# Optimization experiments

Measured on AMD Instinct MI355X. Metric: run time of the kernel, lower is better.

Reference implementation:

```python
import jax, jax.numpy as jnp
import numpy as np

B, S, D, H = 2, 2048, 1024, 16
DK = D // H


def setup_inputs() -> dict:
    key = jax.random.key(0)
    ks = jax.random.split(key, 14)
    inp = {
        'query': jax.random.normal(ks[0], (B, S, D), jnp.float32),
        'key': jax.random.normal(ks[1], (B, S, D), jnp.float32),
        'value': jax.random.normal(ks[2], (B, S, D), jnp.float32),
        'mask': jax.random.randint(ks[3], (B, 1, S, S), 0, 2).astype(bool),
        'rel_pos_bias': jax.random.normal(ks[4], (1, H, S, S), jnp.float32),
    }
    scale = 1.0 / np.sqrt(D)
    names = ['Wq', 'bq', 'Wk', 'bk', 'Wv', 'bv', 'Wo', 'bo']
    for i, n in enumerate(names):
        k = ks[5 + i]
        if n.startswith('W'):
            inp[n] = jax.random.normal(k, (D, D), jnp.float32) * scale
        else:
            inp[n] = jnp.zeros((D,), jnp.float32)
    return inp


def reference(query, key, value, mask, rel_pos_bias, Wq, bq, Wk, bk, Wv, bv, Wo, bo):
    # torch Linear: y = x @ W^T + b; W stored [out, in]
    def proj(x, W, b):
        y = x @ W.T + b                       # [B,S,D]
        return y.reshape(B, S, H, DK).transpose(0, 2, 1, 3)  # [B,H,S,DK]

    q = proj(query, Wq, bq)
    k = proj(key, Wk, bk)
    v = proj(value, Wv, bv)

    scores = jnp.einsum('bhqd,bhkd->bhqk', q, k) / jnp.sqrt(jnp.float32(DK))
    scores = scores + rel_pos_bias
    scores = jnp.where(mask, jnp.float32(-1e9), scores)
    p_attn = jax.nn.softmax(scores, axis=-1)
    x = jnp.einsum('bhqk,bhkd->bhqd', p_attn, v)  # [B,H,S,DK]
    x = x.transpose(0, 2, 1, 3).reshape(B, S, D)
    return x @ Wo.T + bo
```

## Files before the change

kernel.cpp:

```cpp
#include <hip/hip_runtime.h>
#include <stdint.h>


typedef _Float16 f16;
typedef _Float16 f16x8 __attribute__((ext_vector_type(8)));
typedef _Float16 f16x4 __attribute__((ext_vector_type(4)));
typedef float f32x4 __attribute__((ext_vector_type(4)));

#define LOG2E 1.44269504088896340736f

__device__ __forceinline__ void gload16(const void* g, void* l) {
  __builtin_amdgcn_global_load_lds(
      (const __attribute__((address_space(1))) unsigned int*)g,
      (__attribute__((address_space(3))) unsigned int*)l, 16, 0, 0);
}

__global__ __launch_bounds__(256) void cvt_f32_f16(const float* __restrict__ in,
                                                   f16* __restrict__ out, int n4) {
  const int i = blockIdx.x * 256 + threadIdx.x;
  if (i >= n4) return;
  const float4 v = ((const float4*)in)[i];
  f16x4 o = {(f16)v.x, (f16)v.y, (f16)v.z, (f16)v.w};
  ((f16x4*)out)[i] = o;
}

__global__ void mask_detect(const uint8_t* __restrict__ m, int* __restrict__ flag) {
  __shared__ int s_off, s_weird;
  const int t = threadIdx.x;
  if (t == 0) { s_off = 0; s_weird = 0; }
  __syncthreads();
  int f_off = 0, f_weird = 0;
  for (int i = t; i < 8192; i += 256) {
    const uint8_t v = m[i];
    if ((i & 3) && v) f_off = 1;
    if (v > 1) f_weird = 1;
  }
  if (f_off) atomicOr(&s_off, 1);
  if (f_weird) atomicOr(&s_weird, 1);
  __syncthreads();
  if (t == 0) *flag = (s_off && !s_weird) ? 1 : 0;
}

__global__ __launch_bounds__(256) void mask_canon(const uint8_t* __restrict__ m,
                                                  uint8_t* __restrict__ out,
                                                  const int* __restrict__ flag) {
  const int i = (blockIdx.x * 256 + threadIdx.x) * 4;
  uchar4 o;
  if (*flag) {
    const uchar4 v = *(const uchar4*)(m + i);
    o = make_uchar4(v.x != 0, v.y != 0, v.z != 0, v.w != 0);
  } else {
    const int4 v = *(const int4*)((const int*)m + i);
    o = make_uchar4(v.x != 0, v.y != 0, v.z != 0, v.w != 0);
  }
  *(uchar4*)(out + i) = o;
}

template <int MODE>
__global__ __launch_bounds__(256, 2) void gemm_bt(const f16* __restrict__ A,
                                                  const f16* __restrict__ Bw,
                                                  const float* __restrict__ bias,
                                                  void* __restrict__ outp,
                                                  float scale) {
  constexpr int K = 1024;
  const int t = threadIdx.x;
  const int w = t >> 6, lane = t & 63, l15 = lane & 15, l4 = lane >> 4;
  const int bm = (int)(blockIdx.x >> 4) * 128;
  const int bn = (int)(blockIdx.x & 15) * 64;

  __shared__ f16 As[2][128 * 32];
  __shared__ f16 Bs[2][64 * 32];

  const f16* a0 = A + (size_t)(bm + (t >> 2)) * K + (t & 3) * 8;
  const f16* a1 = a0 + (size_t)64 * K;
  const f16* b0 = Bw + (size_t)(bn + (t >> 2)) * K + (t & 3) * 8;

  f32x4 acc[2][4];
#pragma unroll
  for (int m = 0; m < 2; ++m)
#pragma unroll
    for (int n = 0; n < 4; ++n) acc[m][n] = (f32x4){0.f, 0.f, 0.f, 0.f};

#define STAGE_G(buf, k0)                          \
  do {                                            \
    gload16(a0 + (k0), &As[buf][w * 512]);        \
    gload16(a1 + (k0), &As[buf][2048 + w * 512]); \
    gload16(b0 + (k0), &Bs[buf][w * 512]);        \
  } while (0)

  STAGE_G(0, 0);
  __syncthreads();
  int cur = 0;
#pragma unroll 1
  for (int kt = 0; kt < 32; ++kt) {
    if (kt < 31) STAGE_G(cur ^ 1, (kt + 1) * 32);
    const f16* ap = &As[cur][(w * 32 + l15) * 32 + l4 * 8];
    const f16* bp = &Bs[cur][l15 * 32 + l4 * 8];
    f16x8 af[2], bfr[4];
#pragma unroll
    for (int m = 0; m < 2; ++m) af[m] = *(const f16x8*)(ap + m * 512);
#pragma unroll
    for (int n = 0; n < 4; ++n) bfr[n] = *(const f16x8*)(bp + n * 512);
#pragma unroll
    for (int m = 0; m < 2; ++m)
#pragma unroll
      for (int n = 0; n < 4; ++n)
        acc[m][n] = __builtin_amdgcn_mfma_f32_16x16x32_f16(af[m], bfr[n], acc[m][n], 0, 0, 0);
    __syncthreads();
    cur ^= 1;
  }
#undef STAGE_G

#pragma unroll
  for (int m = 0; m < 2; ++m) {
    const int r0 = bm + w * 32 + m * 16 + (l4 << 2);
#pragma unroll
    for (int n = 0; n < 4; ++n) {
      const int c = bn + n * 16 + l15;
      const float bv = bias[c];
#pragma unroll
      for (int j = 0; j < 4; ++j) {
        const int r = r0 + j;
        const float v = (acc[m][n][j] + bv) * scale;
        if (MODE == 0) {
          const int b_ = r >> 11, s = r & 2047, h_ = c >> 6, dk = c & 63;
          ((f16*)outp)[(((size_t)b_ * 16 + h_) * 2048 + s) * 64 + dk] = (f16)v;
        } else if (MODE == 1) {
          const int b_ = r >> 11, s = r & 2047, h_ = c >> 6, dk = c & 63;
          ((f16*)outp)[(((size_t)b_ * 16 + h_) * 64 + dk) * 2048 + s] = (f16)v;
        } else {
          ((float*)outp)[(size_t)r * 1024 + c] = v;
        }
      }
    }
  }
}

__device__ __forceinline__ const f16x8* swzr(const f16* base, int row, int bytecol) {
  return (const f16x8*)((const char*)base + row * 128 + (bytecol ^ ((row & 7) << 4)));
}

__global__ __launch_bounds__(256, 4) void attn_fwd(
    const f16* __restrict__ Qp, const f16* __restrict__ Kp,
    const f16* __restrict__ Vt, const float* __restrict__ bias,
    const uint8_t* __restrict__ mask, f16* __restrict__ X) {
  constexpr int S = 2048;
  const int bid = blockIdx.x;
  const int qt = bid & 31, b = (bid >> 5) & 1, h = bid >> 6;
  const int t = threadIdx.x, w = t >> 6, lane = t & 63;
  const int l15 = lane & 15, l4 = lane >> 4;
  const int q0 = qt * 64 + w * 16;

  const f16* Qbh = Qp + (size_t)(b * 16 + h) * S * 64;
  const f16* Kbh = Kp + (size_t)(b * 16 + h) * S * 64;
  const f16* Vbh = Vt + (size_t)(b * 16 + h) * 64 * S;
  const float* biasr = bias + (size_t)h * S * S + (size_t)(q0 + l15) * S + l4 * 4;
  const uint8_t* maskr = mask + (size_t)b * S * S + (size_t)(q0 + l15) * S + l4 * 4;

  __shared__ f16 Ks[2][64 * 64];
  __shared__ f16 Vs[2][64 * 64];
  __shared__ f16 Ps[4][16 * 64];

  f16x8 qf[2];
#pragma unroll
  for (int ks = 0; ks < 2; ++ks)
    qf[ks] = *(const f16x8*)(Qbh + (size_t)(q0 + l15) * 64 + ks * 32 + l4 * 8);

  f32x4 oacc[4];
#pragma unroll
  for (int n = 0; n < 4; ++n) oacc[n] = (f32x4){0.f, 0.f, 0.f, 0.f};
  float mrow = -3e38f, lrow = 0.f;

  const int srow = t >> 3;
  const int scol = (((t & 7) ^ (srow & 7)) << 3);

#define STAGE(bf, kk)                                                              \
  do {                                                                             \
    gload16(Kbh + (size_t)((kk) + srow) * 64 + scol, &Ks[bf][w * 512]);            \
    gload16(Kbh + (size_t)((kk) + 32 + srow) * 64 + scol, &Ks[bf][2048 + w * 512]);\
    gload16(Vbh + (size_t)srow * S + (kk) + scol, &Vs[bf][w * 512]);               \
    gload16(Vbh + (size_t)(32 + srow) * S + (kk) + scol, &Vs[bf][2048 + w * 512]); \
  } while (0)

  STAGE(0, 0);
  f32x4 bcur[4];
  uint32_t mcur[4];
#pragma unroll
  for (int n = 0; n < 4; ++n) {
    bcur[n] = *(const f32x4*)(biasr + n * 16);
    mcur[n] = *(const uint32_t*)(maskr + n * 16);
  }
  __syncthreads();

  int buf = 0;
#pragma unroll 1
  for (int kt = 0; kt < 32; ++kt) {
    const int k0 = kt * 64;
    f32x4 bnxt[4];
    uint32_t mnxt[4];
    if (kt < 31) {
      STAGE(buf ^ 1, k0 + 64);
#pragma unroll
      for (int n = 0; n < 4; ++n) {
        bnxt[n] = *(const f32x4*)(biasr + k0 + 64 + n * 16);
        mnxt[n] = *(const uint32_t*)(maskr + k0 + 64 + n * 16);
      }
    }

    f32x4 sacc[4];
#pragma unroll
    for (int n = 0; n < 4; ++n) sacc[n] = (f32x4){0.f, 0.f, 0.f, 0.f};
#pragma unroll
    for (int n = 0; n < 4; ++n)
#pragma unroll
      for (int ks = 0; ks < 2; ++ks) {
        const f16x8 kf = *swzr(&Ks[buf][0], n * 16 + l15, ks * 64 + l4 * 16);
        sacc[n] = __builtin_amdgcn_mfma_f32_16x16x32_f16(kf, qf[ks], sacc[n], 0, 0, 0);
      }

    float tmax = -3e38f;
#pragma unroll
    for (int n = 0; n < 4; ++n)
#pragma unroll
      for (int j = 0; j < 4; ++j) {
        float s = fmaf(bcur[n][j], LOG2E, sacc[n][j]);
        s = ((mcur[n] >> (8 * j)) & 255u) ? -1.44269504e9f : s;
        sacc[n][j] = s;
        tmax = fmaxf(tmax, s);
      }
    tmax = fmaxf(tmax, __shfl_xor(tmax, 16));
    tmax = fmaxf(tmax, __shfl_xor(tmax, 32));

    const float mnew = fmaxf(mrow, tmax);
    const float alpha = __builtin_exp2f(mrow - mnew);
    mrow = mnew;
    float lsum = 0.f;
#pragma unroll
    for (int n = 0; n < 4; ++n)
#pragma unroll
      for (int j = 0; j < 4; ++j) {
        const float e = __builtin_exp2f(sacc[n][j] - mnew);
        sacc[n][j] = e;
        lsum += e;
      }
    lsum += __shfl_xor(lsum, 16);
    lsum += __shfl_xor(lsum, 32);
    lrow = lrow * alpha + lsum;

    float aq[4];
#pragma unroll
    for (int j = 0; j < 4; ++j) aq[j] = __shfl(alpha, l4 * 4 + j);
#pragma unroll
    for (int n = 0; n < 4; ++n)
#pragma unroll
      for (int j = 0; j < 4; ++j) oacc[n][j] *= aq[j];

#pragma unroll
    for (int n = 0; n < 4; ++n) {
      f16x4 pk = {(f16)sacc[n][0], (f16)sacc[n][1], (f16)sacc[n][2], (f16)sacc[n][3]};
      *(f16x4*)((char*)&Ps[w][0] + l15 * 128 +
                ((32 * n + 8 * l4) ^ ((l15 & 7) << 4))) = pk;
    }

    f16x8 pf[2];
#pragma unroll
    for (int ks = 0; ks < 2; ++ks) pf[ks] = *swzr(&Ps[w][0], l15, ks * 64 + l4 * 16);
#pragma unroll
    for (int ks = 0; ks < 2; ++ks)
#pragma unroll
      for (int n = 0; n < 4; ++n) {
        const f16x8 vf = *swzr(&Vs[buf][0], n * 16 + l15, ks * 64 + l4 * 16);
        oacc[n] = __builtin_amdgcn_mfma_f32_16x16x32_f16(pf[ks], vf, oacc[n], 0, 0, 0);
      }

    __syncthreads();
    buf ^= 1;
    if (kt < 31) {
#pragma unroll
      for (int n = 0; n < 4; ++n) { bcur[n] = bnxt[n]; mcur[n] = mnxt[n]; }
    }
  }
#undef STAGE

  const float inv = 1.0f / lrow;
  float invq[4];
#pragma unroll
  for (int j = 0; j < 4; ++j) invq[j] = __shfl(inv, l4 * 4 + j);
#pragma unroll
  for (int j = 0; j < 4; ++j) {
    const int qrow = q0 + l4 * 4 + j;
#pragma unroll
    for (int n = 0; n < 4; ++n)
      X[((size_t)b * 2048 + qrow) * 1024 + h * 64 + n * 16 + l15] =
          (f16)(oacc[n][j] * invq[j]);
  }
}

extern "C" void kernel_launch(void* const* d_in, const int* in_sizes, int n_in,
                              void* d_out, int out_size, void* d_ws, size_t ws_size,
                              hipStream_t stream) {
  const float* query = (const float*)d_in[0];
  const float* key_ = (const float*)d_in[1];
  const float* value = (const float*)d_in[2];
  const uint8_t* mask = (const uint8_t*)d_in[3];
  const float* bias = (const float*)d_in[4];
  const float* Wq = (const float*)d_in[5];
  const float* bq = (const float*)d_in[6];
  const float* Wk = (const float*)d_in[7];
  const float* bk = (const float*)d_in[8];
  const float* Wv = (const float*)d_in[9];
  const float* bv = (const float*)d_in[10];
  const float* Wo = (const float*)d_in[11];
  const float* bo = (const float*)d_in[12];

  char* p = (char*)d_ws;
  f16* qh = (f16*)p; p += (size_t)4194304 * 2;
  f16* kh = (f16*)p; p += (size_t)4194304 * 2;
  f16* vh = (f16*)p; p += (size_t)4194304 * 2;
  f16* wqh = (f16*)p; p += (size_t)1048576 * 2;
  f16* wkh = (f16*)p; p += (size_t)1048576 * 2;
  f16* wvh = (f16*)p; p += (size_t)1048576 * 2;
  f16* woh = (f16*)p; p += (size_t)1048576 * 2;
  f16* Qp = (f16*)p; p += (size_t)4194304 * 2;
  f16* Kp = (f16*)p; p += (size_t)4194304 * 2;
  f16* Vt = (f16*)p; p += (size_t)4194304 * 2;
  f16* Xh = (f16*)p; p += (size_t)4194304 * 2;
  uint8_t* m8 = (uint8_t*)p; p += (size_t)8388608;
  int* flag = (int*)p; p += 256;
  if (ws_size < (size_t)(p - (char*)d_ws)) return;

  mask_detect<<<1, 256, 0, stream>>>(mask, flag);
  mask_canon<<<8192, 256, 0, stream>>>(mask, m8, flag);

  cvt_f32_f16<<<4096, 256, 0, stream>>>(query, qh, 1048576);
  cvt_f32_f16<<<4096, 256, 0, stream>>>(key_, kh, 1048576);
  cvt_f32_f16<<<4096, 256, 0, stream>>>(value, vh, 1048576);
  cvt_f32_f16<<<1024, 256, 0, stream>>>(Wq, wqh, 262144);
  cvt_f32_f16<<<1024, 256, 0, stream>>>(Wk, wkh, 262144);
  cvt_f32_f16<<<1024, 256, 0, stream>>>(Wv, wvh, 262144);
  cvt_f32_f16<<<1024, 256, 0, stream>>>(Wo, woh, 262144);

  gemm_bt<0><<<512, 256, 0, stream>>>(qh, wqh, bq, Qp, 0.125f * LOG2E);
  gemm_bt<0><<<512, 256, 0, stream>>>(kh, wkh, bk, Kp, 1.0f);
  gemm_bt<1><<<512, 256, 0, stream>>>(vh, wvh, bv, Vt, 1.0f);

  attn_fwd<<<1024, 256, 0, stream>>>(Qp, Kp, Vt, bias, m8, Xh);

  gemm_bt<2><<<512, 256, 0, stream>>>(Xh, woh, bo, d_out, 1.0f);
}
```

Baseline: 310.8 us.

## Batch conversions and QKV GEMMs into single launches; deepen attention K/V prefetch

```diff
diff --git a/kernel.cpp b/kernel.cpp
--- a/kernel.cpp
+++ b/kernel.cpp
@@ -15,11 +15,14 @@
       (__attribute__((address_space(3))) unsigned int*)l, 16, 0, 0);
 }
 
-__global__ __launch_bounds__(256) void cvt_f32_f16(const float* __restrict__ in,
-                                                   f16* __restrict__ out, int n4) {
+struct CvtSrcs { const float* s[7]; };
+
+__global__ __launch_bounds__(256) void cvt_all(CvtSrcs a, f16* __restrict__ out) {
   const int i = blockIdx.x * 256 + threadIdx.x;
-  if (i >= n4) return;
-  const float4 v = ((const float4*)in)[i];
+  int r, base;
+  if (i < 3145728) { r = i >> 20; base = r << 20; }
+  else { r = 3 + ((i - 3145728) >> 18); base = 3145728 + ((r - 3) << 18); }
+  const float4 v = ((const float4*)a.s[r])[i - base];
   f16x4 o = {(f16)v.x, (f16)v.y, (f16)v.z, (f16)v.w};
   ((f16x4*)out)[i] = o;
 }
@@ -56,17 +59,21 @@
   *(uchar4*)(out + i) = o;
 }
 
-template <int MODE>
-__global__ __launch_bounds__(256, 2) void gemm_bt(const f16* __restrict__ A,
-                                                  const f16* __restrict__ Bw,
-                                                  const float* __restrict__ bias,
-                                                  void* __restrict__ outp,
-                                                  float scale) {
+__global__ __launch_bounds__(256, 2) void gemm_qkv(
+    const f16* __restrict__ qh, const f16* __restrict__ kh, const f16* __restrict__ vh,
+    const f16* __restrict__ wq, const f16* __restrict__ wk, const f16* __restrict__ wv,
+    const float* __restrict__ bq, const float* __restrict__ bk, const float* __restrict__ bv,
+    f16* __restrict__ Qp, f16* __restrict__ Kp, f16* __restrict__ Vt) {
   constexpr int K = 1024;
   const int t = threadIdx.x;
   const int w = t >> 6, lane = t & 63, l15 = lane & 15, l4 = lane >> 4;
-  const int bm = (int)(blockIdx.x >> 4) * 128;
-  const int bn = (int)(blockIdx.x & 15) * 64;
+  const int nt = (int)blockIdx.x % 48;
+  const int bm = ((int)blockIdx.x / 48) * 128;
+  const int which = nt >> 4;
+  const int bn = (nt & 15) * 64;
+  const f16* A = which == 0 ? qh : which == 1 ? kh : vh;
+  const f16* Bw = which == 0 ? wq : which == 1 ? wk : wv;
+  const float* bias = which == 0 ? bq : which == 1 ? bk : bv;
 
   __shared__ f16 As[2][128 * 32];
   __shared__ f16 Bs[2][64 * 32];
@@ -111,6 +118,8 @@
   }
 #undef STAGE_G
 
+  const float scale = which == 0 ? 0.125f * LOG2E : 1.0f;
+  f16* outp = which == 0 ? Qp : which == 1 ? Kp : Vt;
 #pragma unroll
   for (int m = 0; m < 2; ++m) {
     const int r0 = bm + w * 32 + m * 16 + (l4 << 2);
@@ -122,16 +131,79 @@
       for (int j = 0; j < 4; ++j) {
         const int r = r0 + j;
         const float v = (acc[m][n][j] + bv) * scale;
-        if (MODE == 0) {
-          const int b_ = r >> 11, s = r & 2047, h_ = c >> 6, dk = c & 63;
-          ((f16*)outp)[(((size_t)b_ * 16 + h_) * 2048 + s) * 64 + dk] = (f16)v;
-        } else if (MODE == 1) {
-          const int b_ = r >> 11, s = r & 2047, h_ = c >> 6, dk = c & 63;
-          ((f16*)outp)[(((size_t)b_ * 16 + h_) * 64 + dk) * 2048 + s] = (f16)v;
-        } else {
-          ((float*)outp)[(size_t)r * 1024 + c] = v;
-        }
+        const int b_ = r >> 11, s = r & 2047, h_ = c >> 6, dk = c & 63;
+        if (which < 2)
+          outp[(((size_t)b_ * 16 + h_) * 2048 + s) * 64 + dk] = (f16)v;
+        else
+          outp[(((size_t)b_ * 16 + h_) * 64 + dk) * 2048 + s] = (f16)v;
       }
+    }
+  }
+}
+
+__global__ __launch_bounds__(256, 2) void gemm_out(const f16* __restrict__ A,
+                                                   const f16* __restrict__ Bw,
+                                                   const float* __restrict__ bias,
+                                                   float* __restrict__ outp) {
+  constexpr int K = 1024;
+  const int t = threadIdx.x;
+  const int w = t >> 6, lane = t & 63, l15 = lane & 15, l4 = lane >> 4;
+  const int bm = (int)(blockIdx.x >> 4) * 128;
+  const int bn = (int)(blockIdx.x & 15) * 64;
+
+  __shared__ f16 As[2][128 * 32];
+  __shared__ f16 Bs[2][64 * 32];
+
+  const f16* a0 = A + (size_t)(bm + (t >> 2)) * K + (t & 3) * 8;
+  const f16* a1 = a0 + (size_t)64 * K;
+  const f16* b0 = Bw + (size_t)(bn + (t >> 2)) * K + (t & 3) * 8;
+
+  f32x4 acc[2][4];
+#pragma unroll
+  for (int m = 0; m < 2; ++m)
+#pragma unroll
+    for (int n = 0; n < 4; ++n) acc[m][n] = (f32x4){0.f, 0.f, 0.f, 0.f};
+
+#define STAGE_G(buf, k0)                          \
+  do {                                            \
+    gload16(a0 + (k0), &As[buf][w * 512]);        \
+    gload16(a1 + (k0), &As[buf][2048 + w * 512]); \
+    gload16(b0 + (k0), &Bs[buf][w * 512]);        \
+  } while (0)
+
+  STAGE_G(0, 0);
+  __syncthreads();
+  int cur = 0;
+#pragma unroll 1
+  for (int kt = 0; kt < 32; ++kt) {
+    if (kt < 31) STAGE_G(cur ^ 1, (kt + 1) * 32);
+    const f16* ap = &As[cur][(w * 32 + l15) * 32 + l4 * 8];
+    const f16* bp = &Bs[cur][l15 * 32 + l4 * 8];
+    f16x8 af[2], bfr[4];
+#pragma unroll
+    for (int m = 0; m < 2; ++m) af[m] = *(const f16x8*)(ap + m * 512);
+#pragma unroll
+    for (int n = 0; n < 4; ++n) bfr[n] = *(const f16x8*)(bp + n * 512);
+#pragma unroll
+    for (int m = 0; m < 2; ++m)
+#pragma unroll
+      for (int n = 0; n < 4; ++n)
+        acc[m][n] = __builtin_amdgcn_mfma_f32_16x16x32_f16(af[m], bfr[n], acc[m][n], 0, 0, 0);
+    __syncthreads();
+    cur ^= 1;
+  }
+#undef STAGE_G
+
+#pragma unroll
+  for (int m = 0; m < 2; ++m) {
+    const int r0 = bm + w * 32 + m * 16 + (l4 << 2);
+#pragma unroll
+    for (int n = 0; n < 4; ++n) {
+      const int c = bn + n * 16 + l15;
+      const float bv = bias[c];
+#pragma unroll
+      for (int j = 0; j < 4; ++j)
+        outp[(size_t)(r0 + j) * 1024 + c] = acc[m][n][j] + bv;
     }
   }
 }
@@ -174,37 +246,30 @@
   const int srow = t >> 3;
   const int scol = (((t & 7) ^ (srow & 7)) << 3);
 
-#define STAGE(bf, kk)                                                              \
-  do {                                                                             \
-    gload16(Kbh + (size_t)((kk) + srow) * 64 + scol, &Ks[bf][w * 512]);            \
-    gload16(Kbh + (size_t)((kk) + 32 + srow) * 64 + scol, &Ks[bf][2048 + w * 512]);\
-    gload16(Vbh + (size_t)srow * S + (kk) + scol, &Vs[bf][w * 512]);               \
-    gload16(Vbh + (size_t)(32 + srow) * S + (kk) + scol, &Vs[bf][2048 + w * 512]); \
+#define STAGE(bf, kk)                                                               \
+  do {                                                                              \
+    gload16(Kbh + (size_t)((kk) + srow) * 64 + scol, &Ks[bf][w * 512]);             \
+    gload16(Kbh + (size_t)((kk) + 32 + srow) * 64 + scol, &Ks[bf][2048 + w * 512]); \
+    gload16(Vbh + (size_t)srow * S + (kk) + scol, &Vs[bf][w * 512]);                \
+    gload16(Vbh + (size_t)(32 + srow) * S + (kk) + scol, &Vs[bf][2048 + w * 512]);  \
   } while (0)
 
   STAGE(0, 0);
-  f32x4 bcur[4];
-  uint32_t mcur[4];
-#pragma unroll
-  for (int n = 0; n < 4; ++n) {
-    bcur[n] = *(const f32x4*)(biasr + n * 16);
-    mcur[n] = *(const uint32_t*)(maskr + n * 16);
-  }
-  __syncthreads();
-
-  int buf = 0;
+  STAGE(1, 64);
+
 #pragma unroll 1
   for (int kt = 0; kt < 32; ++kt) {
     const int k0 = kt * 64;
-    f32x4 bnxt[4];
-    uint32_t mnxt[4];
-    if (kt < 31) {
-      STAGE(buf ^ 1, k0 + 64);
-#pragma unroll
-      for (int n = 0; n < 4; ++n) {
-        bnxt[n] = *(const f32x4*)(biasr + k0 + 64 + n * 16);
-        mnxt[n] = *(const uint32_t*)(maskr + k0 + 64 + n * 16);
-      }
+    const int buf = kt & 1;
+    asm volatile("s_waitcnt vmcnt(4)" ::: "memory");
+    __builtin_amdgcn_s_barrier();
+
+    f32x4 bc[4];
+    uint32_t mc[4];
+#pragma unroll
+    for (int n = 0; n < 4; ++n) {
+      bc[n] = *(const f32x4*)(biasr + k0 + n * 16);
+      mc[n] = *(const uint32_t*)(maskr + k0 + n * 16);
     }
 
     f32x4 sacc[4];
@@ -223,8 +288,8 @@
     for (int n = 0; n < 4; ++n)
 #pragma unroll
       for (int j = 0; j < 4; ++j) {
-        float s = fmaf(bcur[n][j], LOG2E, sacc[n][j]);
-        s = ((mcur[n] >> (8 * j)) & 255u) ? -1.44269504e9f : s;
+        float s = fmaf(bc[n][j], LOG2E, sacc[n][j]);
+        s = ((mc[n] >> (8 * j)) & 255u) ? -1.44269504e9f : s;
         sacc[n][j] = s;
         tmax = fmaxf(tmax, s);
       }
@@ -273,14 +338,12 @@
         oacc[n] = __builtin_amdgcn_mfma_f32_16x16x32_f16(pf[ks], vf, oacc[n], 0, 0, 0);
       }
 
-    __syncthreads();
-    buf ^= 1;
-    if (kt < 31) {
-#pragma unroll
-      for (int n = 0; n < 4; ++n) { bcur[n] = bnxt[n]; mcur[n] = mnxt[n]; }
-    }
+    __builtin_amdgcn_s_barrier();
+    STAGE(buf, (k0 + 128) & (S - 1));
   }
 #undef STAGE
+
+  asm volatile("s_waitcnt vmcnt(0)" ::: "memory");
 
   const float inv = 1.0f / lrow;
   float invq[4];
@@ -332,19 +395,15 @@
   mask_detect<<<1, 256, 0, stream>>>(mask, flag);
   mask_canon<<<8192, 256, 0, stream>>>(mask, m8, flag);
 
-  cvt_f32_f16<<<4096, 256, 0, stream>>>(query, qh, 1048576);
-  cvt_f32_f16<<<4096, 256, 0, stream>>>(key_, kh, 1048576);
-  cvt_f32_f16<<<4096, 256, 0, stream>>>(value, vh, 1048576);
-  cvt_f32_f16<<<1024, 256, 0, stream>>>(Wq, wqh, 262144);
-  cvt_f32_f16<<<1024, 256, 0, stream>>>(Wk, wkh, 262144);
-  cvt_f32_f16<<<1024, 256, 0, stream>>>(Wv, wvh, 262144);
-  cvt_f32_f16<<<1024, 256, 0, stream>>>(Wo, woh, 262144);
-
-  gemm_bt<0><<<512, 256, 0, stream>>>(qh, wqh, bq, Qp, 0.125f * LOG2E);
-  gemm_bt<0><<<512, 256, 0, stream>>>(kh, wkh, bk, Kp, 1.0f);
-  gemm_bt<1><<<512, 256, 0, stream>>>(vh, wvh, bv, Vt, 1.0f);
+  CvtSrcs cs;
+  cs.s[0] = query; cs.s[1] = key_; cs.s[2] = value;
+  cs.s[3] = Wq; cs.s[4] = Wk; cs.s[5] = Wv; cs.s[6] = Wo;
+  cvt_all<<<16384, 256, 0, stream>>>(cs, qh);
+
+  gemm_qkv<<<1536, 256, 0, stream>>>(qh, kh, vh, wqh, wkh, wvh, bq, bk, bv,
+                                     Qp, Kp, Vt);
 
   attn_fwd<<<1024, 256, 0, stream>>>(Qp, Kp, Vt, bias, m8, Xh);
 
-  gemm_bt<2><<<512, 256, 0, stream>>>(Xh, woh, bo, d_out, 1.0f);
-}
+  gemm_out<<<512, 256, 0, stream>>>(Xh, woh, bo, (float*)d_out);
+}
```

Result: faster. 288.5 us (-7.2%).
